# Kernel tuning notes

Hardware: AMD Instinct MI355X
Metric: run time of the kernel (lower is better)

The kernel has to match this reference:

```python
import jax, jax.numpy as jnp
import numpy as np

B, F, E, H = 4096, 26, 64, 1000000
D = F * E  # 1664

def setup_inputs() -> dict:
    key = jax.random.key(0)
    ks = jax.random.split(key, 12)
    s = 0.02  # init scale
    return {
        "ids": jax.random.randint(ks[0], (B, F), 0, H),
        "emb": jax.random.normal(ks[1], (H, E), jnp.float32) * s,
        "cross_w": jax.random.normal(ks[2], (3, D), jnp.float32) * s,
        "cross_b": jnp.zeros((3, D), jnp.float32),
        "w1": jax.random.normal(ks[3], (D, 1024), jnp.float32) * s,
        "b1": jnp.zeros((1024,), jnp.float32),
        "w2": jax.random.normal(ks[4], (1024, 512), jnp.float32) * s,
        "b2": jnp.zeros((512,), jnp.float32),
        "w3": jax.random.normal(ks[5], (512, 256), jnp.float32) * s,
        "b3": jnp.zeros((256,), jnp.float32),
        "out_w": jax.random.normal(ks[6], (D + 256, 1), jnp.float32) * s,
        "out_b": jnp.zeros((), jnp.float32),
    }

def reference(ids, emb, cross_w, cross_b, w1, b1, w2, b2, w3, b3, out_w, out_b):
    # Embedding lookup + field-wise concat -> x0: [B, D]
    x0 = emb[ids].reshape(ids.shape[0], -1)
    # Cross net. Original materializes [B,D,D] outer product x0 * x^T then
    # giving the same math with O(B*D) memory.
    x = x0
    for i in range(cross_w.shape[0]):
        s = x @ cross_w[i]                 # [B] per-example scalar
        x = x0 * s[:, None] + cross_b[i] + x
    # Deep tower on x0
    h = jax.nn.relu(x0 @ w1 + b1)
    h = jax.nn.relu(h @ w2 + b2)
    h = jax.nn.relu(h @ w3 + b3)
    # Output head
    logit = jnp.concatenate([x, h], axis=1) @ out_w + out_b  # [B, 1]
    return jax.nn.sigmoid(logit)
```

## Files before the change

kernel.cpp:

```cpp
#include <hip/hip_runtime.h>
#include <hip/hip_bf16.h>

#define B_  4096
#define F_  26
#define E_  64
#define D_  1664
#define N1_ 1024
#define N2_ 512
#define N3_ 256

typedef __attribute__((ext_vector_type(8))) __bf16 bf16x8;
typedef __attribute__((ext_vector_type(4))) float  f32x4;

__device__ __forceinline__ unsigned short f2b(float x) {
    __hip_bfloat16 h = __float2bfloat16(x);
    return __builtin_bit_cast(unsigned short, h);
}
__device__ __forceinline__ float b2f(unsigned short u) {
    return __uint_as_float(((unsigned)u) << 16);
}

__device__ __forceinline__ void async_load16(const void* g, void* l) {
    __builtin_amdgcn_global_load_lds(
        (const __attribute__((address_space(1))) void*)g,
        (__attribute__((address_space(3))) void*)l,
        16, 0, 0);
}

__device__ __forceinline__ f32x4 mfma16(bf16x8 a, bf16x8 b, f32x4 c) {
    return __builtin_amdgcn_mfma_f32_16x16x32_bf16(a, b, c, 0, 0, 0);
}

__global__ __launch_bounds__(256) void gather_cross_kernel(
        const int* __restrict__ ids, const float* __restrict__ emb,
        const float* __restrict__ cw, const float* __restrict__ cb,
        const float* __restrict__ out_w,
        unsigned short* __restrict__ x0b, float* __restrict__ partial)
{
    __shared__ int   sid[F_];
    __shared__ float red[4];
    const int b = blockIdx.x;
    const int t = threadIdx.x;
    const int lane = t & 63, w = t >> 6;

    if (t < F_) sid[t] = ids[b * F_ + t];
    __syncthreads();

    float x0r[7], xv[7];
    #pragma unroll
    for (int j = 0; j < 7; j++) {
        const int d = t + j * 256;
        float v = 0.f;
        if (d < D_) {
            const int f = d >> 6;
            v = emb[(size_t)sid[f] * E_ + (d & 63)];
            x0b[(size_t)b * D_ + d] = f2b(v);
        }
        x0r[j] = v; xv[j] = v;
    }
    for (int i = 0; i < 3; i++) {
        float s = 0.f;
        #pragma unroll
        for (int j = 0; j < 7; j++) {
            const int d = t + j * 256;
            if (d < D_) s += xv[j] * cw[i * D_ + d];
        }
        #pragma unroll
        for (int off = 32; off > 0; off >>= 1) s += __shfl_down(s, off, 64);
        __syncthreads();
        if (lane == 0) red[w] = s;
        __syncthreads();
        const float st = red[0] + red[1] + red[2] + red[3];
        #pragma unroll
        for (int j = 0; j < 7; j++) {
            const int d = t + j * 256;
            if (d < D_) xv[j] = x0r[j] * st + cb[i * D_ + d] + xv[j];
        }
    }
    float s = 0.f;
    #pragma unroll
    for (int j = 0; j < 7; j++) {
        const int d = t + j * 256;
        if (d < D_) s += xv[j] * out_w[d];
    }
    #pragma unroll
    for (int off = 32; off > 0; off >>= 1) s += __shfl_down(s, off, 64);
    __syncthreads();
    if (lane == 0) red[w] = s;
    __syncthreads();
    if (t == 0) partial[b] = red[0] + red[1] + red[2] + red[3];
}

__global__ __launch_bounds__(256) void transpose_cast_kernel(
        const float* __restrict__ in, unsigned short* __restrict__ out,
        int K, int N)
{
    __shared__ float tile[32][33];
    const int n0 = blockIdx.x * 32, k0 = blockIdx.y * 32;
    const int tc = threadIdx.x & 31, tr = threadIdx.x >> 5;
    #pragma unroll
    for (int p = 0; p < 4; p++)
        tile[tr + p * 8][tc] = in[(size_t)(k0 + tr + p * 8) * N + n0 + tc];
    __syncthreads();
    #pragma unroll
    for (int p = 0; p < 4; p++) {
        const int n = tr + p * 8;
        out[(size_t)(n0 + n) * K + k0 + tc] = f2b(tile[tc][n]);
    }
}

template<int BM, int BN>
__global__ __launch_bounds__(256, 4) void gemm_bias_relu(
        const unsigned short* __restrict__ A,
        const unsigned short* __restrict__ Bt,
        const float* __restrict__ bias,
        unsigned short* __restrict__ C,
        int M, int N, int K)
{
    constexpr int WM = BM / 2, WN = BN / 2;
    constexpr int TI = WM / 16, TJ = WN / 16;
    constexpr int nA = BM / 16, nB = BN / 16, nAB = nA + nB;
    constexpr int TOTC = 2 * nAB;

    __shared__ unsigned short sA[2 * BM * 32];
    __shared__ unsigned short sB[2 * BN * 32];

    const int t    = threadIdx.x;
    const int lane = t & 63;
    const int w    = t >> 6;

    const int i    = blockIdx.y * gridDim.x + blockIdx.x;
    const int xcd  = i & 7;
    const int s    = i >> 3;
    const int ypg  = gridDim.y >> 3;
    const int ty   = xcd * ypg + s / gridDim.x;
    const int tx   = s - (s / gridDim.x) * gridDim.x;
    const int m0   = ty * BM;
    const int n0   = tx * BN;
    const int wm   = (w >> 1) * WM;
    const int wn   = (w & 1) * WN;

    const int srow = lane >> 2;
    const int scol = (lane & 3) * 8;

    f32x4 acc[TI][TJ] = {};

    for (int k0 = 0; k0 < K; k0 += 64) {
        #pragma unroll
        for (int c0 = 0; c0 < TOTC; c0 += 4) {
            const int c = c0 + w;
            const int u = c / nAB;
            const int r = c - u * nAB;
            if (r < nA) {
                const unsigned short* g =
                    A + (size_t)(m0 + r * 16 + srow) * K + k0 + u * 32 + scol;
                async_load16(g, &sA[u * BM * 32 + r * 512]);
            } else {
                const int rb = r - nA;
                const unsigned short* g =
                    Bt + (size_t)(n0 + rb * 16 + srow) * K + k0 + u * 32 + scol;
                async_load16(g, &sB[u * BN * 32 + rb * 512]);
            }
        }
        __syncthreads();

        #pragma unroll
        for (int u = 0; u < 2; u++) {
            bf16x8 af[TI], bf[TJ];
            #pragma unroll
            for (int ii = 0; ii < TI; ii++)
                af[ii] = *(const bf16x8*)
                    &sA[u * BM * 32 + (wm + ii * 16 + (lane & 15)) * 32 + (lane >> 4) * 8];
            #pragma unroll
            for (int j = 0; j < TJ; j++)
                bf[j] = *(const bf16x8*)
                    &sB[u * BN * 32 + (wn + j * 16 + (lane & 15)) * 32 + (lane >> 4) * 8];
            #pragma unroll
            for (int ii = 0; ii < TI; ii++)
                #pragma unroll
                for (int j = 0; j < TJ; j++)
                    acc[ii][j] = mfma16(af[ii], bf[j], acc[ii][j]);
        }
        __syncthreads();
    }

    #pragma unroll
    for (int ii = 0; ii < TI; ii++) {
        const int r0 = m0 + wm + ii * 16 + (lane >> 4) * 4;
        #pragma unroll
        for (int j = 0; j < TJ; j++) {
            const int col = n0 + wn + j * 16 + (lane & 15);
            const float bv = bias[col];
            #pragma unroll
            for (int r = 0; r < 4; r++) {
                float v = acc[ii][j][r] + bv;
                v = fmaxf(v, 0.f);
                C[(size_t)(r0 + r) * N + col] = f2b(v);
            }
        }
    }
}

__global__ __launch_bounds__(256) void head_kernel(
        const float* __restrict__ partial, const unsigned short* __restrict__ h3,
        const float* __restrict__ out_w, const float* __restrict__ out_b,
        float* __restrict__ out)
{
    const int gw   = (blockIdx.x * 256 + threadIdx.x) >> 6;
    const int lane = threadIdx.x & 63;
    if (gw >= B_) return;
    float s = 0.f;
    #pragma unroll
    for (int q = 0; q < 4; q++) {
        const int j = lane + q * 64;
        s += b2f(h3[(size_t)gw * N3_ + j]) * out_w[D_ + j];
    }
    #pragma unroll
    for (int off = 32; off > 0; off >>= 1) s += __shfl_down(s, off, 64);
    if (lane == 0) {
        const float logit = partial[gw] + s + out_b[0];
        out[gw] = 1.f / (1.f + expf(-logit));
    }
}

extern "C" void kernel_launch(void* const* d_in, const int* in_sizes, int n_in,
                              void* d_out, int out_size, void* d_ws, size_t ws_size,
                              hipStream_t stream)
{
    (void)in_sizes; (void)n_in; (void)out_size; (void)ws_size;
    const int*   ids     = (const int*)  d_in[0];
    const float* emb     = (const float*)d_in[1];
    const float* cross_w = (const float*)d_in[2];
    const float* cross_b = (const float*)d_in[3];
    const float* w1      = (const float*)d_in[4];
    const float* b1      = (const float*)d_in[5];
    const float* w2      = (const float*)d_in[6];
    const float* b2      = (const float*)d_in[7];
    const float* w3      = (const float*)d_in[8];
    const float* b3      = (const float*)d_in[9];
    const float* out_w   = (const float*)d_in[10];
    const float* out_b   = (const float*)d_in[11];
    float* out = (float*)d_out;

    char* p = (char*)d_ws;
    auto alloc = [&](size_t bytes) {
        char* r = p; p += (bytes + 255) & ~(size_t)255; return r;
    };
    unsigned short* x0b = (unsigned short*)alloc((size_t)B_ * D_ * 2);
    unsigned short* w1t = (unsigned short*)alloc((size_t)D_ * N1_ * 2);
    unsigned short* w2t = (unsigned short*)alloc((size_t)N1_ * N2_ * 2);
    unsigned short* w3t = (unsigned short*)alloc((size_t)N2_ * N3_ * 2);
    unsigned short* h1  = (unsigned short*)alloc((size_t)B_ * N1_ * 2);
    unsigned short* h2  = (unsigned short*)alloc((size_t)B_ * N2_ * 2);
    unsigned short* h3  = (unsigned short*)alloc((size_t)B_ * N3_ * 2);
    float* partial      = (float*)alloc((size_t)B_ * 4);

    gather_cross_kernel<<<B_, 256, 0, stream>>>(
        ids, emb, cross_w, cross_b, out_w, x0b, partial);
    transpose_cast_kernel<<<dim3(N1_ / 32, D_  / 32), 256, 0, stream>>>(w1, w1t, D_,  N1_);
    transpose_cast_kernel<<<dim3(N2_ / 32, N1_ / 32), 256, 0, stream>>>(w2, w2t, N1_, N2_);
    transpose_cast_kernel<<<dim3(N3_ / 32, N2_ / 32), 256, 0, stream>>>(w3, w3t, N2_, N3_);

    gemm_bias_relu<64, 64><<<dim3(N1_ / 64, B_ / 64), 256, 0, stream>>>(
        x0b, w1t, b1, h1, B_, N1_, D_);
    gemm_bias_relu<64, 32><<<dim3(N2_ / 32, B_ / 64), 256, 0, stream>>>(
        h1, w2t, b2, h2, B_, N2_, N1_);
    gemm_bias_relu<32, 32><<<dim3(N3_ / 32, B_ / 32), 256, 0, stream>>>(
        h2, w3t, b3, h3, B_, N3_, N2_);

    head_kernel<<<B_ / 4, 256, 0, stream>>>(partial, h3, out_w, out_b, out);
}
```

Measured before the change: 385.9 us.

## Pre-pack operands into MFMA fragment layout and stream GEMMs without LDS

Activations and weights are written directly in a 32x32x16 MFMA fragment-packed layout, so each GEMM wave loads its operand fragments straight from global memory with 16-byte loads and needs no shared-memory staging or barriers. The three transpose kernels are merged into one pack kernel. The GEMMs move to 32x32x16 MFMA tiles and write packed outputs through an LDS epilogue. The gather/cross kernel is vectorised to float4 loads. In exchange, each wave has no cross-wave data reuse through LDS, which adds L2 traffic and leaves global load latency exposed without an explicit pipeline.

```diff
diff --git a/kernel.cpp b/kernel.cpp
--- a/kernel.cpp
+++ b/kernel.cpp
@@ -9,8 +9,9 @@
 #define N2_ 512
 #define N3_ 256
 
-typedef __attribute__((ext_vector_type(8))) __bf16 bf16x8;
-typedef __attribute__((ext_vector_type(4))) float  f32x4;
+typedef __attribute__((ext_vector_type(8)))  __bf16         bf16x8;
+typedef __attribute__((ext_vector_type(8)))  unsigned short u16x8;
+typedef __attribute__((ext_vector_type(16))) float          f32x16;
 
 __device__ __forceinline__ unsigned short f2b(float x) {
     __hip_bfloat16 h = __float2bfloat16(x);
@@ -20,50 +21,48 @@
     return __uint_as_float(((unsigned)u) << 16);
 }
 
-__device__ __forceinline__ void async_load16(const void* g, void* l) {
-    __builtin_amdgcn_global_load_lds(
-        (const __attribute__((address_space(1))) void*)g,
-        (__attribute__((address_space(3))) void*)l,
-        16, 0, 0);
-}
-
-__device__ __forceinline__ f32x4 mfma16(bf16x8 a, bf16x8 b, f32x4 c) {
-    return __builtin_amdgcn_mfma_f32_16x16x32_bf16(a, b, c, 0, 0, 0);
-}
 
 __global__ __launch_bounds__(256) void gather_cross_kernel(
         const int* __restrict__ ids, const float* __restrict__ emb,
         const float* __restrict__ cw, const float* __restrict__ cb,
         const float* __restrict__ out_w,
-        unsigned short* __restrict__ x0b, float* __restrict__ partial)
+        u16x8* __restrict__ x0p, float* __restrict__ partial)
 {
     __shared__ int   sid[F_];
     __shared__ float red[4];
     const int b = blockIdx.x;
     const int t = threadIdx.x;
     const int lane = t & 63, w = t >> 6;
+    const bool act = (t < 208);
 
     if (t < F_) sid[t] = ids[b * F_ + t];
     __syncthreads();
 
-    float x0r[7], xv[7];
-    #pragma unroll
-    for (int j = 0; j < 7; j++) {
-        const int d = t + j * 256;
-        float v = 0.f;
-        if (d < D_) {
-            const int f = d >> 6;
-            v = emb[(size_t)sid[f] * E_ + (d & 63)];
-            x0b[(size_t)b * D_ + d] = f2b(v);
-        }
-        x0r[j] = v; xv[j] = v;
+    const float4* emb4 = (const float4*)emb;
+    const float4* cw4  = (const float4*)cw;
+    const float4* cb4  = (const float4*)cb;
+    const float4* ow4  = (const float4*)out_w;
+
+    float4 x00 = make_float4(0,0,0,0), x01 = x00, xv0 = x00, xv1 = x00;
+    if (act) {
+        const int f  = t >> 3;
+        const int c0 = 2 * t;
+        x00 = emb4[(size_t)sid[f] * 16 + (c0 & 15)];
+        x01 = emb4[(size_t)sid[f] * 16 + ((c0 + 1) & 15)];
+        u16x8 o;
+        o[0]=f2b(x00.x); o[1]=f2b(x00.y); o[2]=f2b(x00.z); o[3]=f2b(x00.w);
+        o[4]=f2b(x01.x); o[5]=f2b(x01.y); o[6]=f2b(x01.z); o[7]=f2b(x01.w);
+        const int mt = b >> 5, ks = t >> 1, ls = (b & 31) + 32 * (t & 1);
+        x0p[((size_t)mt * 104 + ks) * 64 + ls] = o;
+        xv0 = x00; xv1 = x01;
     }
     for (int i = 0; i < 3; i++) {
         float s = 0.f;
-        #pragma unroll
-        for (int j = 0; j < 7; j++) {
-            const int d = t + j * 256;
-            if (d < D_) s += xv[j] * cw[i * D_ + d];
+        if (act) {
+            const float4 wa = cw4[i * 416 + 2 * t];
+            const float4 wb = cw4[i * 416 + 2 * t + 1];
+            s = xv0.x*wa.x + xv0.y*wa.y + xv0.z*wa.z + xv0.w*wa.w
+              + xv1.x*wb.x + xv1.y*wb.y + xv1.z*wb.z + xv1.w*wb.w;
         }
         #pragma unroll
         for (int off = 32; off > 0; off >>= 1) s += __shfl_down(s, off, 64);
@@ -71,17 +70,21 @@
         if (lane == 0) red[w] = s;
         __syncthreads();
         const float st = red[0] + red[1] + red[2] + red[3];
-        #pragma unroll
-        for (int j = 0; j < 7; j++) {
-            const int d = t + j * 256;
-            if (d < D_) xv[j] = x0r[j] * st + cb[i * D_ + d] + xv[j];
+        if (act) {
+            const float4 ba = cb4[i * 416 + 2 * t];
+            const float4 bb = cb4[i * 416 + 2 * t + 1];
+            xv0.x = x00.x*st + ba.x + xv0.x;  xv0.y = x00.y*st + ba.y + xv0.y;
+            xv0.z = x00.z*st + ba.z + xv0.z;  xv0.w = x00.w*st + ba.w + xv0.w;
+            xv1.x = x01.x*st + bb.x + xv1.x;  xv1.y = x01.y*st + bb.y + xv1.y;
+            xv1.z = x01.z*st + bb.z + xv1.z;  xv1.w = x01.w*st + bb.w + xv1.w;
         }
     }
     float s = 0.f;
-    #pragma unroll
-    for (int j = 0; j < 7; j++) {
-        const int d = t + j * 256;
-        if (d < D_) s += xv[j] * out_w[d];
+    if (act) {
+        const float4 wa = ow4[2 * t];
+        const float4 wb = ow4[2 * t + 1];
+        s = xv0.x*wa.x + xv0.y*wa.y + xv0.z*wa.z + xv0.w*wa.w
+          + xv1.x*wb.x + xv1.y*wb.y + xv1.z*wb.z + xv1.w*wb.w;
     }
     #pragma unroll
     for (int off = 32; off > 0; off >>= 1) s += __shfl_down(s, off, 64);
@@ -91,113 +94,117 @@
     if (t == 0) partial[b] = red[0] + red[1] + red[2] + red[3];
 }
 
-__global__ __launch_bounds__(256) void transpose_cast_kernel(
-        const float* __restrict__ in, unsigned short* __restrict__ out,
-        int K, int N)
-{
-    __shared__ float tile[32][33];
-    const int n0 = blockIdx.x * 32, k0 = blockIdx.y * 32;
-    const int tc = threadIdx.x & 31, tr = threadIdx.x >> 5;
-    #pragma unroll
-    for (int p = 0; p < 4; p++)
-        tile[tr + p * 8][tc] = in[(size_t)(k0 + tr + p * 8) * N + n0 + tc];
-    __syncthreads();
-    #pragma unroll
-    for (int p = 0; p < 4; p++) {
-        const int n = tr + p * 8;
-        out[(size_t)(n0 + n) * K + k0 + tc] = f2b(tile[tc][n]);
-    }
-}
-
-template<int BM, int BN>
-__global__ __launch_bounds__(256, 4) void gemm_bias_relu(
-        const unsigned short* __restrict__ A,
-        const unsigned short* __restrict__ Bt,
-        const float* __restrict__ bias,
-        unsigned short* __restrict__ C,
-        int M, int N, int K)
-{
-    constexpr int WM = BM / 2, WN = BN / 2;
-    constexpr int TI = WM / 16, TJ = WN / 16;
-    constexpr int nA = BM / 16, nB = BN / 16, nAB = nA + nB;
-    constexpr int TOTC = 2 * nAB;
-
-    __shared__ unsigned short sA[2 * BM * 32];
-    __shared__ unsigned short sB[2 * BN * 32];
-
-    const int t    = threadIdx.x;
-    const int lane = t & 63;
-    const int w    = t >> 6;
-
-    const int i    = blockIdx.y * gridDim.x + blockIdx.x;
-    const int xcd  = i & 7;
-    const int s    = i >> 3;
-    const int ypg  = gridDim.y >> 3;
-    const int ty   = xcd * ypg + s / gridDim.x;
-    const int tx   = s - (s / gridDim.x) * gridDim.x;
-    const int m0   = ty * BM;
-    const int n0   = tx * BN;
-    const int wm   = (w >> 1) * WM;
-    const int wn   = (w & 1) * WN;
-
-    const int srow = lane >> 2;
-    const int scol = (lane & 3) * 8;
-
-    f32x4 acc[TI][TJ] = {};
-
-    for (int k0 = 0; k0 < K; k0 += 64) {
-        #pragma unroll
-        for (int c0 = 0; c0 < TOTC; c0 += 4) {
-            const int c = c0 + w;
-            const int u = c / nAB;
-            const int r = c - u * nAB;
-            if (r < nA) {
-                const unsigned short* g =
-                    A + (size_t)(m0 + r * 16 + srow) * K + k0 + u * 32 + scol;
-                async_load16(g, &sA[u * BM * 32 + r * 512]);
-            } else {
-                const int rb = r - nA;
-                const unsigned short* g =
-                    Bt + (size_t)(n0 + rb * 16 + srow) * K + k0 + u * 32 + scol;
-                async_load16(g, &sB[u * BN * 32 + rb * 512]);
+__global__ __launch_bounds__(256) void pack_weights_kernel(
+        const float* __restrict__ w1, const float* __restrict__ w2,
+        const float* __restrict__ w3,
+        u16x8* __restrict__ p1, u16x8* __restrict__ p2, u16x8* __restrict__ p3)
+{
+    __shared__ float tile[128][33];
+    const int bid = blockIdx.x;
+    const float* in; u16x8* out; int N, ntiles, KS;
+    int tl;
+    if (bid < 416)      { in = w1; out = p1; N = N1_; ntiles = 32; KS = 104; tl = bid; }
+    else if (bid < 544) { in = w2; out = p2; N = N2_; ntiles = 16; KS = 64;  tl = bid - 416; }
+    else                { in = w3; out = p3; N = N3_; ntiles = 8;  KS = 32;  tl = bid - 544; }
+    const int nt = tl % ntiles;
+    const int kg = tl / ntiles;
+    const int t  = threadIdx.x;
+
+    #pragma unroll
+    for (int p = 0; p < 16; p++) {
+        const int row = p * 8 + (t >> 5);
+        tile[row][t & 31] = in[(size_t)(kg * 128 + row) * N + nt * 32 + (t & 31)];
+    }
+    __syncthreads();
+    #pragma unroll
+    for (int q = 0; q < 2; q++) {
+        const int idx = q * 256 + t;
+        const int ksl = idx >> 6, l = idx & 63;
+        const int kr  = ksl * 16 + (l >> 5) * 8;
+        u16x8 o;
+        #pragma unroll
+        for (int e = 0; e < 8; e++) o[e] = f2b(tile[kr + e][l & 31]);
+        out[((size_t)nt * KS + kg * 8 + ksl) * 64 + l] = o;
+    }
+}
+
+template<int TI, int TJ, int KS, bool PACK_OUT>
+__global__ __launch_bounds__(256) void stream_gemm(
+        const u16x8* __restrict__ Ap, const u16x8* __restrict__ Bp,
+        const float* __restrict__ bias, void* __restrict__ Cout,
+        int N, int KSo)
+{
+    const int t = threadIdx.x, lane = t & 63, w = t >> 6;
+    const int wy = w >> 1, wx = w & 1;
+
+    const int i   = blockIdx.y * gridDim.x + blockIdx.x;
+    const int xcd = i & 7, s = i >> 3;
+    const int ypg = gridDim.y >> 3;
+    const int by  = xcd * ypg + s / gridDim.x;
+    const int bx  = s % gridDim.x;
+    const int mt0 = (by * 2 + wy) * TI;
+    const int nt0 = (bx * 2 + wx) * TJ;
+
+    f32x16 acc[TI][TJ] = {};
+
+    #pragma unroll 4
+    for (int ks = 0; ks < KS; ks++) {
+        bf16x8 af[TI], bf[TJ];
+        #pragma unroll
+        for (int a = 0; a < TI; a++)
+            af[a] = __builtin_bit_cast(bf16x8,
+                Ap[((size_t)(mt0 + a) * KS + ks) * 64 + lane]);
+        #pragma unroll
+        for (int b = 0; b < TJ; b++)
+            bf[b] = __builtin_bit_cast(bf16x8,
+                Bp[((size_t)(nt0 + b) * KS + ks) * 64 + lane]);
+        #pragma unroll
+        for (int a = 0; a < TI; a++)
+            #pragma unroll
+            for (int b = 0; b < TJ; b++)
+                acc[a][b] = __builtin_amdgcn_mfma_f32_32x32x16_bf16(
+                    af[a], bf[b], acc[a][b], 0, 0, 0);
+    }
+
+    if (PACK_OUT) {
+        constexpr int PITCH = TJ * 32 + 8;
+        __shared__ __align__(16) unsigned short lt[4 * TI * 32 * PITCH];
+        unsigned short* L = lt + w * TI * 32 * PITCH;
+        #pragma unroll
+        for (int a = 0; a < TI; a++)
+            #pragma unroll
+            for (int b = 0; b < TJ; b++) {
+                const float bv = bias[(nt0 + b) * 32 + (lane & 31)];
+                #pragma unroll
+                for (int r = 0; r < 16; r++) {
+                    const int row_l = a * 32 + (r & 3) + 8 * (r >> 2) + 4 * (lane >> 5);
+                    const int col_l = b * 32 + (lane & 31);
+                    L[row_l * PITCH + col_l] = f2b(fmaxf(acc[a][b][r] + bv, 0.f));
+                }
             }
-        }
-        __syncthreads();
-
-        #pragma unroll
-        for (int u = 0; u < 2; u++) {
-            bf16x8 af[TI], bf[TJ];
-            #pragma unroll
-            for (int ii = 0; ii < TI; ii++)
-                af[ii] = *(const bf16x8*)
-                    &sA[u * BM * 32 + (wm + ii * 16 + (lane & 15)) * 32 + (lane >> 4) * 8];
-            #pragma unroll
-            for (int j = 0; j < TJ; j++)
-                bf[j] = *(const bf16x8*)
-                    &sB[u * BN * 32 + (wn + j * 16 + (lane & 15)) * 32 + (lane >> 4) * 8];
-            #pragma unroll
-            for (int ii = 0; ii < TI; ii++)
+        u16x8* Co = (u16x8*)Cout;
+        #pragma unroll
+        for (int a = 0; a < TI; a++)
+            #pragma unroll
+            for (int ksl = 0; ksl < TJ * 2; ksl++) {
+                const u16x8 v = *(const u16x8*)
+                    &L[(a * 32 + (lane & 31)) * PITCH + ksl * 16 + (lane >> 5) * 8];
+                Co[((size_t)(mt0 + a) * KSo + (nt0 * 2 + ksl)) * 64 + lane] = v;
+            }
+    } else {
+        unsigned short* Co = (unsigned short*)Cout;
+        #pragma unroll
+        for (int a = 0; a < TI; a++)
+            #pragma unroll
+            for (int b = 0; b < TJ; b++) {
+                const int colg = (nt0 + b) * 32 + (lane & 31);
+                const float bv = bias[colg];
                 #pragma unroll
-                for (int j = 0; j < TJ; j++)
-                    acc[ii][j] = mfma16(af[ii], bf[j], acc[ii][j]);
-        }
-        __syncthreads();
-    }
-
-    #pragma unroll
-    for (int ii = 0; ii < TI; ii++) {
-        const int r0 = m0 + wm + ii * 16 + (lane >> 4) * 4;
-        #pragma unroll
-        for (int j = 0; j < TJ; j++) {
-            const int col = n0 + wn + j * 16 + (lane & 15);
-            const float bv = bias[col];
-            #pragma unroll
-            for (int r = 0; r < 4; r++) {
-                float v = acc[ii][j][r] + bv;
-                v = fmaxf(v, 0.f);
-                C[(size_t)(r0 + r) * N + col] = f2b(v);
+                for (int r = 0; r < 16; r++) {
+                    const int rowg = (mt0 + a) * 32 + (r & 3) + 8 * (r >> 2) + 4 * (lane >> 5);
+                    Co[(size_t)rowg * N + colg] = f2b(fmaxf(acc[a][b][r] + bv, 0.f));
+                }
             }
-        }
     }
 }
 
@@ -246,27 +253,25 @@
     auto alloc = [&](size_t bytes) {
         char* r = p; p += (bytes + 255) & ~(size_t)255; return r;
     };
-    unsigned short* x0b = (unsigned short*)alloc((size_t)B_ * D_ * 2);
-    unsigned short* w1t = (unsigned short*)alloc((size_t)D_ * N1_ * 2);
-    unsigned short* w2t = (unsigned short*)alloc((size_t)N1_ * N2_ * 2);
-    unsigned short* w3t = (unsigned short*)alloc((size_t)N2_ * N3_ * 2);
-    unsigned short* h1  = (unsigned short*)alloc((size_t)B_ * N1_ * 2);
-    unsigned short* h2  = (unsigned short*)alloc((size_t)B_ * N2_ * 2);
-    unsigned short* h3  = (unsigned short*)alloc((size_t)B_ * N3_ * 2);
-    float* partial      = (float*)alloc((size_t)B_ * 4);
+    u16x8* x0p = (u16x8*)alloc((size_t)B_ * D_ * 2);
+    u16x8* w1p = (u16x8*)alloc((size_t)D_ * N1_ * 2);
+    u16x8* w2p = (u16x8*)alloc((size_t)N1_ * N2_ * 2);
+    u16x8* w3p = (u16x8*)alloc((size_t)N2_ * N3_ * 2);
+    u16x8* h1p = (u16x8*)alloc((size_t)B_ * N1_ * 2);
+    u16x8* h2p = (u16x8*)alloc((size_t)B_ * N2_ * 2);
+    unsigned short* h3 = (unsigned short*)alloc((size_t)B_ * N3_ * 2);
+    float* partial     = (float*)alloc((size_t)B_ * 4);
 
     gather_cross_kernel<<<B_, 256, 0, stream>>>(
-        ids, emb, cross_w, cross_b, out_w, x0b, partial);
-    transpose_cast_kernel<<<dim3(N1_ / 32, D_  / 32), 256, 0, stream>>>(w1, w1t, D_,  N1_);
-    transpose_cast_kernel<<<dim3(N2_ / 32, N1_ / 32), 256, 0, stream>>>(w2, w2t, N1_, N2_);
-    transpose_cast_kernel<<<dim3(N3_ / 32, N2_ / 32), 256, 0, stream>>>(w3, w3t, N2_, N3_);
-
-    gemm_bias_relu<64, 64><<<dim3(N1_ / 64, B_ / 64), 256, 0, stream>>>(
-        x0b, w1t, b1, h1, B_, N1_, D_);
-    gemm_bias_relu<64, 32><<<dim3(N2_ / 32, B_ / 64), 256, 0, stream>>>(
-        h1, w2t, b2, h2, B_, N2_, N1_);
-    gemm_bias_relu<32, 32><<<dim3(N3_ / 32, B_ / 32), 256, 0, stream>>>(
-        h2, w3t, b3, h3, B_, N3_, N2_);
+        ids, emb, cross_w, cross_b, out_w, x0p, partial);
+    pack_weights_kernel<<<576, 256, 0, stream>>>(w1, w2, w3, w1p, w2p, w3p);
+
+    stream_gemm<2, 2, 104, true><<<dim3(8, 32), 256, 0, stream>>>(
+        x0p, w1p, b1, h1p, N1_, N1_ / 16);
+    stream_gemm<2, 1, 64, true><<<dim3(8, 32), 256, 0, stream>>>(
+        h1p, w2p, b2, h2p, N2_, N2_ / 16);
+    stream_gemm<1, 1, 32, false><<<dim3(4, 64), 256, 0, stream>>>(
+        h2p, w3p, b3, h3, N3_, 0);
 
     head_kernel<<<B_ / 4, 256, 0, stream>>>(partial, h3, out_w, out_b, out);
 }
```

Result: no change. 392.1 us (+1.6%).
